# Optimization experiments

Measured on AMD Instinct MI355X. Metric: run time of the kernel, lower is better.

The kernel has to match this reference:

```python
import jax, jax.numpy as jnp
import numpy as np

B, S, D = 1, 1024, 64
_EPS = 1e-15
_BND = 1.0 - 1e-7  # artanh domain clamp (mirrors geoopt projection)


def _sq(x):
    return jnp.sum(x * x, axis=-1, keepdims=True)


def _nrm(x):
    return jnp.sqrt(_sq(x) + _EPS)


def _normalize(x, axis, eps):
    n = jnp.sqrt(jnp.sum(x * x, axis=axis, keepdims=True))
    return x / jnp.maximum(n, eps)


def _mobius_add(x, y):
    x2, y2 = _sq(x), _sq(y)
    xy = jnp.sum(x * y, axis=-1, keepdims=True)
    num = (1.0 + 2.0 * xy + y2) * x + (1.0 - x2) * y
    den = 1.0 + 2.0 * xy + x2 * y2
    return num / jnp.maximum(den, _EPS)


def _expmap0(u):
    n = _nrm(u)
    return jnp.tanh(n) * u / n


def _logmap0(y):
    n = _nrm(y)
    return jnp.arctanh(jnp.clip(n, 0.0, _BND)) * y / n


def _dist(x, y):
    n = _nrm(_mobius_add(-x, y))[..., 0]
    return 2.0 * jnp.arctanh(jnp.clip(n, 0.0, _BND))


def _logmap(x, y):
    d = _mobius_add(-x, y)
    n = _nrm(d)
    lam = 2.0 / jnp.maximum(1.0 - _sq(x), _EPS)
    return (2.0 / lam) * jnp.arctanh(jnp.clip(n, 0.0, _BND)) * d / n


def _transp0back(x, v):
    return v / jnp.maximum(1.0 - _sq(x), _EPS)


def _forward(q_in, k_in, v_in, Wq, bq, Wk, bk, Wv, bv, Wo, bo,
             tau, gamma, tangent_scale, gumbel_u, v_rand_init):
    q = q_in @ Wq.T + bq
    k = k_in @ Wk.T + bk
    v = v_in @ Wv.T + bv

    q_hyp = _expmap0(q)   # [B,S,D]
    k_hyp = _expmap0(k)

    # all-pairs geodesic distances [B,S,S]
    dist = _dist(q_hyp[:, :, None, :], k_hyp[:, None, :, :])
    min_d = jnp.min(dist, axis=-1, keepdims=True)
    w_un = jnp.exp(-(dist - min_d))                         # unnormalized weights
    w_sum = jnp.sum(w_un, axis=-1, keepdims=True) + 1e-8
    w_probs = w_un / w_sum
    h = jnp.einsum('bqk,bkd->bqd', w_probs, v)

    # Einstein midpoint: weighted Euclidean centroid of pre-map keys -> manifold
    centroid_euc = jnp.einsum('bqk,bkd->bqd', w_un / w_sum, k)
    centroid_hyp = _expmap0(centroid_euc)                   # [B,S,D]

    c2k = _dist(centroid_hyp[:, :, None, :], k_hyp[:, None, :, :])  # [B,S,S]
    wnv = w_un / w_sum
    entropy = -jnp.sum(wnv * jnp.log(wnv + 1e-8), axis=-1, keepdims=True)
    eff_mass = jnp.exp(entropy)
    variance = jnp.sum(wnv * c2k ** 2, axis=-1, keepdims=True)
    tension = variance - tau * eff_mass                     # [B,S,1]

    # matrix-free TPCA power iteration on weighted local tangents
    k_local = _logmap(centroid_hyp[:, :, None, :], k_hyp[:, None, :, :])  # [B,S,S,D]
    weighted_k = k_local * jnp.sqrt(w_un[..., None] + 1e-8)
    v_r = _normalize(v_rand_init, axis=2, eps=1e-12)        # [B,S,D,1]
    for _ in range(3):
        proj = jnp.einsum('bqkd,bqdo->bqko', weighted_k, v_r)
        v_r = jnp.einsum('bqkd,bqko->bqdo', weighted_k, proj)
        v_r = _normalize(v_r, axis=2, eps=1e-12)
    w_proj_local = v_r[..., 0]                              # [B,S,D]
    w_proj_global = _transp0back(centroid_hyp, w_proj_local)

    q_tan = _logmap0(q_hyp)
    c_tan = _logmap0(centroid_hyp)
    fallback = _normalize(q_tan - c_tan, axis=-1, eps=1e-8)
    w_proj = jnp.where(variance > 1e-5, w_proj_global, fallback)

    h_norm = _nrm(h)
    h_comp = jnp.arcsinh(h_norm) * (h / (h_norm + 1e-8))

    # Pitchfork bifurcation (c = 1)
    x = jnp.sum(h_comp * w_proj, axis=-1, keepdims=True)
    diss = (tension > 0).astype(h.dtype)
    h_mag = _nrm(h_comp)
    amplitude = h_mag * jnp.tanh(tension) * diss
    g = -jnp.log(-jnp.log(gumbel_u))                        # gumbel noise, logits = 0
    y_soft = jax.nn.softmax(g / 0.5, axis=-1)
    y_hard = jax.nn.one_hot(jnp.argmax(y_soft, axis=-1), 2, dtype=h.dtype)
    gp = y_soft + jax.lax.stop_gradient(y_hard - y_soft)    # straight-through
    eps_g = (gp[..., 0] - gp[..., 1])[..., None]            # gp @ [1,-1]
    x_star = eps_g * amplitude
    delta_c = jnp.tanh(x_star - x)
    h_prime = h_comp + delta_c * w_proj
    hp_norm = _nrm(h_prime) + 1e-8
    h_pb = h_prime * (jnp.tanh(hp_norm * tangent_scale) / hp_norm)
    h_prime_hyp = _expmap0(h_pb)

    h_out_bif = _logmap0(h_prime_hyp)
    gate = jax.nn.sigmoid(gamma)
    h_fused = (1.0 - gate) * h + gate * h_out_bif
    return h_fused @ Wo.T + bo


def setup_inputs() -> dict:
    key = jax.random.key(0)
    ks = jax.random.split(key, 10)
    std = 0.02
    return {
        'q_in': jax.random.normal(ks[0], (B, S, D), jnp.float32),
        'k_in': jax.random.normal(ks[1], (B, S, D), jnp.float32),
        'v_in': jax.random.normal(ks[2], (B, S, D), jnp.float32),
        'Wq': std * jax.random.normal(ks[3], (D, D), jnp.float32),
        'bq': jnp.zeros((D,), jnp.float32),
        'Wk': std * jax.random.normal(ks[4], (D, D), jnp.float32),
        'bk': jnp.zeros((D,), jnp.float32),
        'Wv': std * jax.random.normal(ks[5], (D, D), jnp.float32),
        'bv': jnp.zeros((D,), jnp.float32),
        'Wo': std * jax.random.normal(ks[6], (D, D), jnp.float32),
        'bo': jnp.zeros((D,), jnp.float32),
        'tau': jnp.float32(5.0),
        'gamma': jnp.float32(0.0),
        'tangent_scale': jnp.float32(0.1),
        'gumbel_u': jax.random.uniform(ks[7], (B, S, 2), jnp.float32, 1e-6, 1.0 - 1e-6),
        'v_rand_init': jax.random.normal(ks[8], (B, S, D, 1), jnp.float32),
    }


def reference(q_in, k_in, v_in, Wq, bq, Wk, bk, Wv, bv, Wo, bo,
              tau, gamma, tangent_scale, gumbel_u, v_rand_init):
    return _forward(q_in, k_in, v_in, Wq, bq, Wk, bk, Wv, bv, Wo, bo,
                    tau, gamma, tangent_scale, gumbel_u, v_rand_init)
```

## Files before the change

### kernel.cpp

```cpp
#include <hip/hip_runtime.h>
#include <hip/hip_fp16.h>
#include <math.h>

#define S 1024
#define D 64
#define BND 0.99999994f
#define FINF 3.4e38f
#define FMA4(acc,s,v) { (acc).x+=(s)*(v).x; (acc).y+=(s)*(v).y; (acc).z+=(s)*(v).z; (acc).w+=(s)*(v).w; }

__device__ __forceinline__ float waveSum(float v){
  #pragma unroll
  for(int o=32;o>0;o>>=1) v += __shfl_xor(v,o,64);
  return v;
}
__device__ __forceinline__ float2 blockSum512_v2(float2 v, float* red){
  #pragma unroll
  for(int o=32;o>0;o>>=1){ v.x+=__shfl_xor(v.x,o,64); v.y+=__shfl_xor(v.y,o,64); }
  const int wid=threadIdx.x>>6;
  __syncthreads();
  if((threadIdx.x&63)==0){ red[wid*2]=v.x; red[wid*2+1]=v.y; }
  __syncthreads();
  float2 s={0.f,0.f};
  #pragma unroll
  for(int k=0;k<8;k++){ s.x+=red[k*2]; s.y+=red[k*2+1]; }
  return s;
}
__device__ __forceinline__ float2 blockMin512_v2(float2 v, float* red){
  #pragma unroll
  for(int o=32;o>0;o>>=1){ v.x=fminf(v.x,__shfl_xor(v.x,o,64)); v.y=fminf(v.y,__shfl_xor(v.y,o,64)); }
  const int wid=threadIdx.x>>6;
  __syncthreads();
  if((threadIdx.x&63)==0){ red[wid*2]=v.x; red[wid*2+1]=v.y; }
  __syncthreads();
  float2 s={red[0],red[1]};
  #pragma unroll
  for(int k=1;k<8;k++){ s.x=fminf(s.x,red[k*2]); s.y=fminf(s.y,red[k*2+1]); }
  return s;
}
__device__ __forceinline__ float distF(float dot, float y2, float x2, float B){
  const float A=1.f-2.f*dot+y2;
  const float den=fmaxf(1.f-2.f*dot+x2*y2,1e-15f);
  const float num2=fmaxf(A*A*x2 + B*B*y2 - 2.f*A*B*dot, 0.f);
  const float nn=sqrtf(num2/(den*den)+1e-15f);
  return 2.f*atanhf(fminf(nn,BND));
}

__global__ __launch_bounds__(64) void k_proj(
  const float* __restrict__ qin, const float* __restrict__ kin, const float* __restrict__ vin,
  const float* __restrict__ Wq, const float* __restrict__ bq,
  const float* __restrict__ Wk, const float* __restrict__ bk,
  const float* __restrict__ Wv, const float* __restrict__ bv,
  const float* __restrict__ vrand,
  float* __restrict__ q_hyp, float* __restrict__ k_hyp, float* __restrict__ kT,
  __half* __restrict__ kTp,
  float* __restrict__ vproj, float* __restrict__ kproj,
  float* __restrict__ q2, float* __restrict__ k2, float* __restrict__ v_r)
{
  const int i = blockIdx.x, d = threadIdx.x;
  __shared__ __align__(16) float lq[D], lk[D], lv[D];
  __shared__ __align__(16) float skh[D];
  lq[d]=qin[i*D+d]; lk[d]=kin[i*D+d]; lv[d]=vin[i*D+d];
  __syncthreads();
  float aq=bq[d], ak=bk[d], av=bv[d];
  const float4* wq4=(const float4*)(Wq + d*D);
  const float4* wk4=(const float4*)(Wk + d*D);
  const float4* wv4=(const float4*)(Wv + d*D);
  #pragma unroll
  for(int e=0;e<16;e++){
    float4 a=wq4[e], b=wk4[e], c=wv4[e];
    aq += lq[4*e]*a.x + lq[4*e+1]*a.y + lq[4*e+2]*a.z + lq[4*e+3]*a.w;
    ak += lk[4*e]*b.x + lk[4*e+1]*b.y + lk[4*e+2]*b.z + lk[4*e+3]*b.w;
    av += lv[4*e]*c.x + lv[4*e+1]*c.y + lv[4*e+2]*c.z + lv[4*e+3]*c.w;
  }
  float nq = sqrtf(waveSum(aq*aq)+1e-15f);
  float qh = tanhf(nq)*aq/nq;
  q_hyp[i*D+d]=qh;
  float q2v = waveSum(qh*qh);
  if(d==0) q2[i]=q2v;
  float nk = sqrtf(waveSum(ak*ak)+1e-15f);
  float kh = tanhf(nk)*ak/nk;
  k_hyp[i*D+d]=kh;
  kT[(size_t)d*S + i]=kh;
  skh[d]=kh;
  float k2v = waveSum(kh*kh);
  if(d==0) k2[i]=k2v;
  vproj[i*D+d]=av;
  kproj[i*D+d]=ak;
  float vr = vrand[i*D+d];
  float nn = sqrtf(waveSum(vr*vr));
  v_r[i*D+d] = vr/fmaxf(nn,1e-12f);
  __syncthreads();
  if(d<32){
    __half2 hp=__floats2half2_rn(skh[2*d], skh[2*d+1]);
    ((__half2*)kTp)[(size_t)d*S + i]=hp;
  }
}

__global__ __launch_bounds__(512,4) void k_wc(
  const float* __restrict__ q_hyp, const float* __restrict__ kT,
  const float* __restrict__ q2a, const float* __restrict__ k2a,
  const float* __restrict__ vproj, const float* __restrict__ kproj,
  float* __restrict__ wbuf, float* __restrict__ wsum, float* __restrict__ effm,
  float* __restrict__ h, float* __restrict__ c_hyp, float* __restrict__ c2)
{
  const int i0=blockIdx.x*2, tid=threadIdx.x;
  __shared__ __align__(16) float qv[2][D];
  __shared__ __align__(16) float wl[2][S];
  __shared__ __align__(16) float4 sA[1024];
  __shared__ __align__(16) float4 sB[1024];
  __shared__ float red[16];
  if(tid<128) qv[tid>>6][tid&63]=q_hyp[i0*D+tid];
  __syncthreads();
  const float x20=q2a[i0], x21=q2a[i0+1];
  const float B0=1.f-x20, B1=1.f-x21;
  const int j0=2*tid;
  float t00=0.f,t01=0.f,t10=0.f,t11=0.f;
  #pragma unroll 8
  for(int d=0;d<64;++d){
    const float2 y=*(const float2*)(kT + (size_t)d*S + j0);
    const float c0=qv[0][d], c1=qv[1][d];
    t00+=y.x*c0; t01+=y.x*c1; t10+=y.y*c0; t11+=y.y*c1;
  }
  const float2 y2p=*(const float2*)(k2a + j0);
  const float ds00=distF(t00,y2p.x,x20,B0);
  const float ds10=distF(t10,y2p.y,x20,B0);
  const float ds01=distF(t01,y2p.x,x21,B1);
  const float ds11=distF(t11,y2p.y,x21,B1);
  float2 mn2={fminf(ds00,ds10), fminf(ds01,ds11)};
  mn2=blockMin512_v2(mn2,red);
  const float w00=expf(mn2.x-ds00), w10=expf(mn2.x-ds10);
  const float w01=expf(mn2.y-ds01), w11=expf(mn2.y-ds11);
  { float2 a={w00,w10}; *(float2*)&wl[0][j0]=a; *(float2*)(wbuf+(size_t)i0*S+j0)=a; }
  { float2 a={w01,w11}; *(float2*)&wl[1][j0]=a; *(float2*)(wbuf+(size_t)(i0+1)*S+j0)=a; }
  float2 s2={w00+w10, w01+w11};
  s2=blockSum512_v2(s2,red);
  const float s0=s2.x+1e-8f, s1=s2.y+1e-8f;
  if(tid==0){ wsum[i0]=s0; wsum[i0+1]=s1; }
  const float inv0=1.f/s0, inv1=1.f/s1;
  float2 e2={0.f,0.f};
  { const float p0=w00*inv0, p1=w10*inv0; e2.x -= p0*logf(p0+1e-8f)+p1*logf(p1+1e-8f); }
  { const float p0=w01*inv1, p1=w11*inv1; e2.y -= p0*logf(p0+1e-8f)+p1*logf(p1+1e-8f); }
  e2=blockSum512_v2(e2,red);
  if(tid==0){ effm[i0]=expf(e2.x); effm[i0+1]=expf(e2.y); }
  const int dq=tid&15, g=tid>>4;
  float* const pA=(float*)sA;
  float* const pB=(float*)sB;
  {
    float4 ah0={0,0,0,0}, ah1={0,0,0,0}, ac0={0,0,0,0}, ac1={0,0,0,0};
    #pragma unroll 4
    for(int jj=0;jj<32;jj++){
      const int j=jj*32+g;
      const float4 yv=((const float4*)(vproj + j*D))[dq];
      const float4 yk=((const float4*)(kproj + j*D))[dq];
      const float u0=wl[0][j], u1=wl[1][j];
      FMA4(ah0,u0,yv); FMA4(ah1,u1,yv);
      FMA4(ac0,u0,yk); FMA4(ac1,u1,yk);
    }
    *(float4*)&pA[(g*2+0)*64+dq*4]=ah0;
    *(float4*)&pA[(g*2+1)*64+dq*4]=ah1;
    *(float4*)&pB[(g*2+0)*64+dq*4]=ac0;
    *(float4*)&pB[(g*2+1)*64+dq*4]=ac1;
  }
  __syncthreads();
  if(tid<128){
    const int q=tid>>6, d=tid&63;
    float hs=0.f, cs=0.f;
    #pragma unroll 8
    for(int gg=0;gg<32;gg++){ hs+=pA[(gg*2+q)*64+d]; cs+=pB[(gg*2+q)*64+d]; }
    const float invq = q ? inv1 : inv0;
    h[(i0+q)*D+d]=hs*invq;
    const float ca=cs*invq;
    const float n=sqrtf(waveSum(ca*ca)+1e-15f);
    const float ch=tanhf(n)*ca/n;
    c_hyp[(i0+q)*D+d]=ch;
    const float c2v=waveSum(ch*ch);
    if(d==0) c2[i0+q]=c2v;
  }
}

__global__ __launch_bounds__(512,4) void k_pmega(
  const float* __restrict__ c_hyp, const float* __restrict__ k_hyp,
  const float* __restrict__ kT, const __half* __restrict__ kTp,
  const float* __restrict__ c2a, const float* __restrict__ k2a,
  const float* __restrict__ wbuf, const float* __restrict__ wsum,
  const float* __restrict__ effm, const float* __restrict__ tau_p,
  const float* __restrict__ h, const float* __restrict__ q_hyp,
  const float* __restrict__ q2a, const float* __restrict__ v_r,
  const float* __restrict__ gu, const float* __restrict__ gamma_p,
  const float* __restrict__ ts_p, const float* __restrict__ Wo,
  const float* __restrict__ bo, float* __restrict__ out)
{
  const int i0=blockIdx.x*2, tid=threadIdx.x;
  __shared__ __align__(16) float cv[2][D];
  __shared__ __align__(16) float vv[2][D];
  __shared__ __align__(16) float aal[2][S];
  __shared__ __align__(16) float bbl[2][S];
  __shared__ __align__(16) float prow[2][S];
  __shared__ __align__(16) float4 sA[1024];
  __shared__ __align__(16) float fus[2][D];
  __shared__ float red[16];
  __shared__ float scd[2];
  float* const pA=(float*)sA;

  if(tid<128){
    const int q=tid>>6, d=tid&63;
    const float ch=c_hyp[i0*D+tid];
    const float vr=v_r[i0*D+tid];
    cv[q][d]=ch; vv[q][d]=vr;
    const float cd=waveSum(ch*vr);
    if(d==0) scd[q]=cd;
  }
  __syncthreads();
  const float x20=c2a[i0], x21=c2a[i0+1];
  const float Bc0=1.f-x20, Bc1=1.f-x21;
  const float mB0=fmaxf(Bc0,1e-15f), mB1=fmaxf(Bc1,1e-15f);
  const float inv0=1.f/wsum[i0], inv1=1.f/wsum[i0+1];
  const int j0=2*tid;
  const int dq=tid&15, g=tid>>4;
  const float tau=tau_p[0];

  float2 var2;
  {
    float u00=0.f,u01=0.f,u10=0.f,u11=0.f;
    #pragma unroll 8
    for(int d=0;d<64;++d){
      const float2 y=*(const float2*)(kT + (size_t)d*S + j0);
      const float c0=cv[0][d], c1=cv[1][d];
      u00+=y.x*c0; u01+=y.x*c1; u10+=y.y*c0; u11+=y.y*c1;
    }
    const float2 y2p=*(const float2*)(k2a + j0);
    const float2 w0=*(const float2*)(wbuf+(size_t)i0*S+j0);
    const float2 w1=*(const float2*)(wbuf+(size_t)(i0+1)*S+j0);
    float var0=0.f, var1=0.f;
    float a00,a10,a01,a11,b00,b10,b01,b11;
    {
      const float A=1.f-2.f*u00+y2p.x;
      const float den=fmaxf(1.f-2.f*u00+x20*y2p.x,1e-15f);
      const float num2=fmaxf(A*A*x20+Bc0*Bc0*y2p.x-2.f*A*Bc0*u00,0.f);
      const float nn=sqrtf(num2/(den*den)+1e-15f);
      const float art=atanhf(fminf(nn,BND));
      var0 += w0.x*inv0*4.f*art*art;
      const float coef=sqrtf(w0.x+1e-8f)*mB0*art/(nn*den);
      a00=-coef*A; b00=coef*Bc0;
    }
    {
      const float A=1.f-2.f*u10+y2p.y;
      const float den=fmaxf(1.f-2.f*u10+x20*y2p.y,1e-15f);
      const float num2=fmaxf(A*A*x20+Bc0*Bc0*y2p.y-2.f*A*Bc0*u10,0.f);
      const float nn=sqrtf(num2/(den*den)+1e-15f);
      const float art=atanhf(fminf(nn,BND));
      var0 += w0.y*inv0*4.f*art*art;
      const float coef=sqrtf(w0.y+1e-8f)*mB0*art/(nn*den);
      a10=-coef*A; b10=coef*Bc0;
    }
    {
      const float A=1.f-2.f*u01+y2p.x;
      const float den=fmaxf(1.f-2.f*u01+x21*y2p.x,1e-15f);
      const float num2=fmaxf(A*A*x21+Bc1*Bc1*y2p.x-2.f*A*Bc1*u01,0.f);
      const float nn=sqrtf(num2/(den*den)+1e-15f);
      const float art=atanhf(fminf(nn,BND));
      var1 += w1.x*inv1*4.f*art*art;
      const float coef=sqrtf(w1.x+1e-8f)*mB1*art/(nn*den);
      a01=-coef*A; b01=coef*Bc1;
    }
    {
      const float A=1.f-2.f*u11+y2p.y;
      const float den=fmaxf(1.f-2.f*u11+x21*y2p.y,1e-15f);
      const float num2=fmaxf(A*A*x21+Bc1*Bc1*y2p.y-2.f*A*Bc1*u11,0.f);
      const float nn=sqrtf(num2/(den*den)+1e-15f);
      const float art=atanhf(fminf(nn,BND));
      var1 += w1.y*inv1*4.f*art*art;
      const float coef=sqrtf(w1.y+1e-8f)*mB1*art/(nn*den);
      a11=-coef*A; b11=coef*Bc1;
    }
    { float2 t={a00,a10}; *(float2*)&aal[0][j0]=t; }
    { float2 t={a01,a11}; *(float2*)&aal[1][j0]=t; }
    { float2 t={b00,b10}; *(float2*)&bbl[0][j0]=t; }
    { float2 t={b01,b11}; *(float2*)&bbl[1][j0]=t; }
    float2 v2={var0,var1};
    var2=blockSum512_v2(v2,red);
  }

  float2 sal2;
  for(int it3=0; it3<3; ++it3){
    float t00=0.f,t01=0.f,t10=0.f,t11=0.f;
    #pragma unroll 8
    for(int dp=0;dp<32;++dp){
      const __half2 h0=((const __half2*)kTp)[(size_t)dp*S + j0];
      const __half2 h1=((const __half2*)kTp)[(size_t)dp*S + j0+1];
      const float2 f0=__half22float2(h0);
      const float2 f1=__half22float2(h1);
      const float2 v0=*(const float2*)&vv[0][2*dp];
      const float2 v1=*(const float2*)&vv[1][2*dp];
      t00 += f0.x*v0.x + f0.y*v0.y;
      t01 += f0.x*v1.x + f0.y*v1.y;
      t10 += f1.x*v0.x + f1.y*v0.y;
      t11 += f1.x*v1.x + f1.y*v1.y;
    }
    {
      const float cd0=scd[0], cd1=scd[1];
      const float2 a0=*(const float2*)&aal[0][j0], b0=*(const float2*)&bbl[0][j0];
      const float2 a1=*(const float2*)&aal[1][j0], b1=*(const float2*)&bbl[1][j0];
      const float p00=a0.x*cd0+b0.x*t00, p10=a0.y*cd0+b0.y*t10;
      const float p01=a1.x*cd1+b1.x*t01, p11=a1.y*cd1+b1.y*t11;
      { float2 t={p00*b0.x, p10*b0.y}; *(float2*)&prow[0][j0]=t; }
      { float2 t={p01*b1.x, p11*b1.y}; *(float2*)&prow[1][j0]=t; }
      float2 s={p00*a0.x+p10*a0.y, p01*a1.x+p11*a1.y};
      sal2=blockSum512_v2(s,red);
    }
    {
      float4 a0={0,0,0,0}, a1={0,0,0,0};
      #pragma unroll 4
      for(int jj=0;jj<32;jj++){
        const int j=jj*32+g;
        const float4 y=((const float4*)(k_hyp + j*D))[dq];
        const float u0=prow[0][j], u1=prow[1][j];
        FMA4(a0,u0,y); FMA4(a1,u1,y);
      }
      *(float4*)&pA[(g*2+0)*64+dq*4]=a0;
      *(float4*)&pA[(g*2+1)*64+dq*4]=a1;
    }
    __syncthreads();
    if(tid<128){
      const int q=tid>>6, d=tid&63;
      float od=(q?sal2.y:sal2.x)*cv[q][d];
      #pragma unroll 8
      for(int gg=0;gg<32;gg++) od += pA[(gg*2+q)*64+d];
      const float nn=sqrtf(waveSum(od*od));
      const float vn=od/fmaxf(nn,1e-12f);
      vv[q][d]=vn;
      const float cd=waveSum(cv[q][d]*vn);
      if(d==0) scd[q]=cd;
    }
    __syncthreads();
  }

  if(tid<128){
    const int q=tid>>6, d=tid&63;
    const int i=i0+q;
    const float vart = q ? var2.y : var2.x;
    const float tns = vart - tau*effm[i];
    const float x2q_c = q ? x21 : x20;
    const float vd=vv[q][d];
    const float hd=h[i*D+d];
    const float qd=q_hyp[i*D+d];
    const float q2=q2a[i];
    const float wpg=vd/fmaxf(1.f-x2q_c,1e-15f);
    const float nq=sqrtf(q2+1e-15f);
    const float qt=atanhf(fminf(nq,BND))*qd/nq;
    const float ncn=sqrtf(x2q_c+1e-15f);
    const float ct=atanhf(fminf(ncn,BND))*cv[q][d]/ncn;
    const float df=qt-ct;
    const float nd=sqrtf(waveSum(df*df));
    const float fb=df/fmaxf(nd,1e-8f);
    const float wp=(vart>1e-5f)?wpg:fb;
    const float hn=sqrtf(waveSum(hd*hd)+1e-15f);
    const float hc=asinhf(hn)*hd/(hn+1e-8f);
    const float x=waveSum(hc*wp);
    const float hmag=sqrtf(waveSum(hc*hc)+1e-15f);
    const float amp=(tns>0.f)? hmag*tanhf(tns) : 0.f;
    const float u0=gu[i*2], u1=gu[i*2+1];
    const float eg=(u0>=u1)?1.f:-1.f;
    const float dc=tanhf(eg*amp - x);
    const float hp=hc+dc*wp;
    const float hpn=sqrtf(waveSum(hp*hp)+1e-15f)+1e-8f;
    const float hpb=hp*(tanhf(hpn*ts_p[0])/hpn);
    const float n2=sqrtf(waveSum(hpb*hpb)+1e-15f);
    const float hyp=tanhf(n2)*hpb/n2;
    const float n3=sqrtf(waveSum(hyp*hyp)+1e-15f);
    const float bif=atanhf(fminf(n3,BND))*hyp/n3;
    const float gate=1.f/(1.f+expf(-gamma_p[0]));
    fus[q][d]=(1.f-gate)*hd + gate*bif;
  }
  __syncthreads();
  if(tid<128){
    const int q=tid>>6, d=tid&63;
    float acc=bo[d];
    const float4* wo4=(const float4*)(Wo + d*D);
    #pragma unroll
    for(int e=0;e<16;e++){
      float4 wv=wo4[e];
      acc += fus[q][4*e]*wv.x + fus[q][4*e+1]*wv.y + fus[q][4*e+2]*wv.z + fus[q][4*e+3]*wv.w;
    }
    out[(i0+q)*D+d]=acc;
  }
}

extern "C" void kernel_launch(void* const* d_in, const int* in_sizes, int n_in,
                              void* d_out, int out_size, void* d_ws, size_t ws_size,
                              hipStream_t stream)
{
  const float* qin=(const float*)d_in[0];
  const float* kin=(const float*)d_in[1];
  const float* vin=(const float*)d_in[2];
  const float* Wq=(const float*)d_in[3];
  const float* bq=(const float*)d_in[4];
  const float* Wk=(const float*)d_in[5];
  const float* bk=(const float*)d_in[6];
  const float* Wv=(const float*)d_in[7];
  const float* bv=(const float*)d_in[8];
  const float* Wo=(const float*)d_in[9];
  const float* bo=(const float*)d_in[10];
  const float* tau=(const float*)d_in[11];
  const float* gamma=(const float*)d_in[12];
  const float* tscale=(const float*)d_in[13];
  const float* gu=(const float*)d_in[14];
  const float* vrand=(const float*)d_in[15];
  float* out=(float*)d_out;

  float* p=(float*)d_ws;
  float* q_hyp=p; p+=S*D;
  float* k_hyp=p; p+=S*D;
  float* kT=p;    p+=S*D;
  float* vproj=p; p+=S*D;
  float* kproj=p; p+=S*D;
  float* v_r=p;   p+=S*D;
  float* h=p;     p+=S*D;
  float* c_hyp=p; p+=S*D;
  float* q2=p;   p+=S;
  float* k2=p;   p+=S;
  float* c2=p;   p+=S;
  float* wsum=p; p+=S;
  float* effm=p; p+=S;
  __half* kTp=(__half*)p; p+=(S*D)/2;
  float* wbuf=p; p+=(size_t)S*S;

  k_proj<<<S,64,0,stream>>>(qin,kin,vin,Wq,bq,Wk,bk,Wv,bv,vrand,
                            q_hyp,k_hyp,kT,kTp,vproj,kproj,q2,k2,v_r);
  k_wc<<<S/2,512,0,stream>>>(q_hyp,kT,q2,k2,vproj,kproj,
                             wbuf,wsum,effm,h,c_hyp,c2);
  k_pmega<<<S/2,512,0,stream>>>(c_hyp,k_hyp,kT,kTp,c2,k2,wbuf,wsum,effm,tau,
                                h,q_hyp,q2,v_r,gu,gamma,tscale,Wo,bo,out);
}
```

Before: 82.55 us.

## Use 1024-thread blocks with one key per thread and interleave v/k projections

Doubles the block size of the weight/centroid and main kernels so that each thread handles one key column instead of two, which doubles the number of waves per query pair and the parallelism available to hide latency. The v and k projections are stored interleaved in one 128-wide buffer, so the weighted-sum pass reads both with one float4 stream and needs one shared reduction buffer. The cost is more reduction partials, more shared memory per block, and heavier register pressure under the 1024-thread launch bound.

```diff
diff --git a/kernel.cpp b/kernel.cpp
--- a/kernel.cpp
+++ b/kernel.cpp
@@ -13,7 +13,7 @@
   for(int o=32;o>0;o>>=1) v += __shfl_xor(v,o,64);
   return v;
 }
-__device__ __forceinline__ float2 blockSum512_v2(float2 v, float* red){
+__device__ __forceinline__ float2 blockSum1024_v2(float2 v, float* red){
   #pragma unroll
   for(int o=32;o>0;o>>=1){ v.x+=__shfl_xor(v.x,o,64); v.y+=__shfl_xor(v.y,o,64); }
   const int wid=threadIdx.x>>6;
@@ -22,10 +22,10 @@
   __syncthreads();
   float2 s={0.f,0.f};
   #pragma unroll
-  for(int k=0;k<8;k++){ s.x+=red[k*2]; s.y+=red[k*2+1]; }
+  for(int k=0;k<16;k++){ s.x+=red[k*2]; s.y+=red[k*2+1]; }
   return s;
 }
-__device__ __forceinline__ float2 blockMin512_v2(float2 v, float* red){
+__device__ __forceinline__ float2 blockMin1024_v2(float2 v, float* red){
   #pragma unroll
   for(int o=32;o>0;o>>=1){ v.x=fminf(v.x,__shfl_xor(v.x,o,64)); v.y=fminf(v.y,__shfl_xor(v.y,o,64)); }
   const int wid=threadIdx.x>>6;
@@ -34,7 +34,7 @@
   __syncthreads();
   float2 s={red[0],red[1]};
   #pragma unroll
-  for(int k=1;k<8;k++){ s.x=fminf(s.x,red[k*2]); s.y=fminf(s.y,red[k*2+1]); }
+  for(int k=1;k<16;k++){ s.x=fminf(s.x,red[k*2]); s.y=fminf(s.y,red[k*2+1]); }
   return s;
 }
 __device__ __forceinline__ float distF(float dot, float y2, float x2, float B){
@@ -52,8 +52,7 @@
   const float* __restrict__ Wv, const float* __restrict__ bv,
   const float* __restrict__ vrand,
   float* __restrict__ q_hyp, float* __restrict__ k_hyp, float* __restrict__ kT,
-  __half* __restrict__ kTp,
-  float* __restrict__ vproj, float* __restrict__ kproj,
+  __half* __restrict__ kTp, float* __restrict__ vk,
   float* __restrict__ q2, float* __restrict__ k2, float* __restrict__ v_r)
 {
   const int i = blockIdx.x, d = threadIdx.x;
@@ -84,8 +83,8 @@
   skh[d]=kh;
   float k2v = waveSum(kh*kh);
   if(d==0) k2[i]=k2v;
-  vproj[i*D+d]=av;
-  kproj[i*D+d]=ak;
+  vk[(size_t)i*128 + d]      = av;
+  vk[(size_t)i*128 + 64 + d] = ak;
   float vr = vrand[i*D+d];
   float nn = sqrtf(waveSum(vr*vr));
   v_r[i*D+d] = vr/fmaxf(nn,1e-12f);
@@ -96,89 +95,84 @@
   }
 }
 
-__global__ __launch_bounds__(512,4) void k_wc(
+__global__ __launch_bounds__(1024,8) void k_wc(
   const float* __restrict__ q_hyp, const float* __restrict__ kT,
   const float* __restrict__ q2a, const float* __restrict__ k2a,
-  const float* __restrict__ vproj, const float* __restrict__ kproj,
+  const float* __restrict__ vk,
   float* __restrict__ wbuf, float* __restrict__ wsum, float* __restrict__ effm,
   float* __restrict__ h, float* __restrict__ c_hyp, float* __restrict__ c2)
 {
   const int i0=blockIdx.x*2, tid=threadIdx.x;
   __shared__ __align__(16) float qv[2][D];
   __shared__ __align__(16) float wl[2][S];
-  __shared__ __align__(16) float4 sA[1024];
-  __shared__ __align__(16) float4 sB[1024];
-  __shared__ float red[16];
+  __shared__ __align__(16) float4 sA[2048];
+  __shared__ float red[32];
   if(tid<128) qv[tid>>6][tid&63]=q_hyp[i0*D+tid];
   __syncthreads();
   const float x20=q2a[i0], x21=q2a[i0+1];
   const float B0=1.f-x20, B1=1.f-x21;
-  const int j0=2*tid;
-  float t00=0.f,t01=0.f,t10=0.f,t11=0.f;
+  const int j=tid;
+  float t0=0.f, t1=0.f;
   #pragma unroll 8
   for(int d=0;d<64;++d){
-    const float2 y=*(const float2*)(kT + (size_t)d*S + j0);
-    const float c0=qv[0][d], c1=qv[1][d];
-    t00+=y.x*c0; t01+=y.x*c1; t10+=y.y*c0; t11+=y.y*c1;
-  }
-  const float2 y2p=*(const float2*)(k2a + j0);
-  const float ds00=distF(t00,y2p.x,x20,B0);
-  const float ds10=distF(t10,y2p.y,x20,B0);
-  const float ds01=distF(t01,y2p.x,x21,B1);
-  const float ds11=distF(t11,y2p.y,x21,B1);
-  float2 mn2={fminf(ds00,ds10), fminf(ds01,ds11)};
-  mn2=blockMin512_v2(mn2,red);
-  const float w00=expf(mn2.x-ds00), w10=expf(mn2.x-ds10);
-  const float w01=expf(mn2.y-ds01), w11=expf(mn2.y-ds11);
-  { float2 a={w00,w10}; *(float2*)&wl[0][j0]=a; *(float2*)(wbuf+(size_t)i0*S+j0)=a; }
-  { float2 a={w01,w11}; *(float2*)&wl[1][j0]=a; *(float2*)(wbuf+(size_t)(i0+1)*S+j0)=a; }
-  float2 s2={w00+w10, w01+w11};
-  s2=blockSum512_v2(s2,red);
+    const float y=kT[(size_t)d*S + j];
+    t0+=y*qv[0][d]; t1+=y*qv[1][d];
+  }
+  const float y2=k2a[j];
+  const float ds0=distF(t0,y2,x20,B0);
+  const float ds1=distF(t1,y2,x21,B1);
+  float2 mn2={ds0,ds1};
+  mn2=blockMin1024_v2(mn2,red);
+  const float w0=expf(mn2.x-ds0);
+  const float w1=expf(mn2.y-ds1);
+  wl[0][j]=w0; wl[1][j]=w1;
+  wbuf[(size_t)i0*S+j]=w0; wbuf[(size_t)(i0+1)*S+j]=w1;
+  float2 s2={w0,w1};
+  s2=blockSum1024_v2(s2,red);
   const float s0=s2.x+1e-8f, s1=s2.y+1e-8f;
   if(tid==0){ wsum[i0]=s0; wsum[i0+1]=s1; }
   const float inv0=1.f/s0, inv1=1.f/s1;
-  float2 e2={0.f,0.f};
-  { const float p0=w00*inv0, p1=w10*inv0; e2.x -= p0*logf(p0+1e-8f)+p1*logf(p1+1e-8f); }
-  { const float p0=w01*inv1, p1=w11*inv1; e2.y -= p0*logf(p0+1e-8f)+p1*logf(p1+1e-8f); }
-  e2=blockSum512_v2(e2,red);
+  float2 e2;
+  { const float p0=w0*inv0, p1=w1*inv1;
+    e2.x = -p0*logf(p0+1e-8f);
+    e2.y = -p1*logf(p1+1e-8f); }
+  e2=blockSum1024_v2(e2,red);
   if(tid==0){ effm[i0]=expf(e2.x); effm[i0+1]=expf(e2.y); }
-  const int dq=tid&15, g=tid>>4;
+  const int dq5=tid&31, g=tid>>5;
   float* const pA=(float*)sA;
-  float* const pB=(float*)sB;
   {
-    float4 ah0={0,0,0,0}, ah1={0,0,0,0}, ac0={0,0,0,0}, ac1={0,0,0,0};
+    float4 a0={0,0,0,0}, a1={0,0,0,0};
     #pragma unroll 4
     for(int jj=0;jj<32;jj++){
-      const int j=jj*32+g;
-      const float4 yv=((const float4*)(vproj + j*D))[dq];
-      const float4 yk=((const float4*)(kproj + j*D))[dq];
-      const float u0=wl[0][j], u1=wl[1][j];
-      FMA4(ah0,u0,yv); FMA4(ah1,u1,yv);
-      FMA4(ac0,u0,yk); FMA4(ac1,u1,yk);
-    }
-    *(float4*)&pA[(g*2+0)*64+dq*4]=ah0;
-    *(float4*)&pA[(g*2+1)*64+dq*4]=ah1;
-    *(float4*)&pB[(g*2+0)*64+dq*4]=ac0;
-    *(float4*)&pB[(g*2+1)*64+dq*4]=ac1;
-  }
-  __syncthreads();
-  if(tid<128){
-    const int q=tid>>6, d=tid&63;
-    float hs=0.f, cs=0.f;
+      const int j2=jj*32+g;
+      const float4 y=((const float4*)(vk + (size_t)j2*128))[dq5];
+      const float u0=wl[0][j2], u1=wl[1][j2];
+      FMA4(a0,u0,y); FMA4(a1,u1,y);
+    }
+    *(float4*)&pA[(g*2+0)*128 + dq5*4]=a0;
+    *(float4*)&pA[(g*2+1)*128 + dq5*4]=a1;
+  }
+  __syncthreads();
+  if(tid<256){
+    const int q=tid>>7, dd=tid&127;
+    float s=0.f;
     #pragma unroll 8
-    for(int gg=0;gg<32;gg++){ hs+=pA[(gg*2+q)*64+d]; cs+=pB[(gg*2+q)*64+d]; }
-    const float invq = q ? inv1 : inv0;
-    h[(i0+q)*D+d]=hs*invq;
-    const float ca=cs*invq;
-    const float n=sqrtf(waveSum(ca*ca)+1e-15f);
-    const float ch=tanhf(n)*ca/n;
-    c_hyp[(i0+q)*D+d]=ch;
-    const float c2v=waveSum(ch*ch);
-    if(d==0) c2[i0+q]=c2v;
-  }
-}
-
-__global__ __launch_bounds__(512,4) void k_pmega(
+    for(int gg=0;gg<32;gg++) s+=pA[(gg*2+q)*128+dd];
+    s *= (q ? inv1 : inv0);
+    if(dd<64){
+      h[(i0+q)*D+dd]=s;
+    }else{
+      const int d=dd-64;
+      const float n=sqrtf(waveSum(s*s)+1e-15f);
+      const float ch=tanhf(n)*s/n;
+      c_hyp[(i0+q)*D+d]=ch;
+      const float c2v=waveSum(ch*ch);
+      if(d==0) c2[i0+q]=c2v;
+    }
+  }
+}
+
+__global__ __launch_bounds__(1024,8) void k_pmega(
   const float* __restrict__ c_hyp, const float* __restrict__ k_hyp,
   const float* __restrict__ kT, const __half* __restrict__ kTp,
   const float* __restrict__ c2a, const float* __restrict__ k2a,
@@ -196,9 +190,9 @@
   __shared__ __align__(16) float aal[2][S];
   __shared__ __align__(16) float bbl[2][S];
   __shared__ __align__(16) float prow[2][S];
-  __shared__ __align__(16) float4 sA[1024];
+  __shared__ __align__(16) float4 sA[2048];
   __shared__ __align__(16) float fus[2][D];
-  __shared__ float red[16];
+  __shared__ float red[32];
   __shared__ float scd[2];
   float* const pA=(float*)sA;
 
@@ -215,106 +209,76 @@
   const float Bc0=1.f-x20, Bc1=1.f-x21;
   const float mB0=fmaxf(Bc0,1e-15f), mB1=fmaxf(Bc1,1e-15f);
   const float inv0=1.f/wsum[i0], inv1=1.f/wsum[i0+1];
-  const int j0=2*tid;
+  const int j=tid;
   const int dq=tid&15, g=tid>>4;
   const float tau=tau_p[0];
 
   float2 var2;
   {
-    float u00=0.f,u01=0.f,u10=0.f,u11=0.f;
+    float u0=0.f, u1=0.f;
     #pragma unroll 8
     for(int d=0;d<64;++d){
-      const float2 y=*(const float2*)(kT + (size_t)d*S + j0);
-      const float c0=cv[0][d], c1=cv[1][d];
-      u00+=y.x*c0; u01+=y.x*c1; u10+=y.y*c0; u11+=y.y*c1;
-    }
-    const float2 y2p=*(const float2*)(k2a + j0);
-    const float2 w0=*(const float2*)(wbuf+(size_t)i0*S+j0);
-    const float2 w1=*(const float2*)(wbuf+(size_t)(i0+1)*S+j0);
-    float var0=0.f, var1=0.f;
-    float a00,a10,a01,a11,b00,b10,b01,b11;
+      const float y=kT[(size_t)d*S + j];
+      u0+=y*cv[0][d]; u1+=y*cv[1][d];
+    }
+    const float y2=k2a[j];
+    const float wq0=wbuf[(size_t)i0*S+j];
+    const float wq1=wbuf[(size_t)(i0+1)*S+j];
+    float var0, var1;
     {
-      const float A=1.f-2.f*u00+y2p.x;
-      const float den=fmaxf(1.f-2.f*u00+x20*y2p.x,1e-15f);
-      const float num2=fmaxf(A*A*x20+Bc0*Bc0*y2p.x-2.f*A*Bc0*u00,0.f);
+      const float A=1.f-2.f*u0+y2;
+      const float den=fmaxf(1.f-2.f*u0+x20*y2,1e-15f);
+      const float num2=fmaxf(A*A*x20+Bc0*Bc0*y2-2.f*A*Bc0*u0,0.f);
       const float nn=sqrtf(num2/(den*den)+1e-15f);
       const float art=atanhf(fminf(nn,BND));
-      var0 += w0.x*inv0*4.f*art*art;
-      const float coef=sqrtf(w0.x+1e-8f)*mB0*art/(nn*den);
-      a00=-coef*A; b00=coef*Bc0;
+      var0 = wq0*inv0*4.f*art*art;
+      const float coef=sqrtf(wq0+1e-8f)*mB0*art/(nn*den);
+      aal[0][j]=-coef*A; bbl[0][j]=coef*Bc0;
     }
     {
-      const float A=1.f-2.f*u10+y2p.y;
-      const float den=fmaxf(1.f-2.f*u10+x20*y2p.y,1e-15f);
-      const float num2=fmaxf(A*A*x20+Bc0*Bc0*y2p.y-2.f*A*Bc0*u10,0.f);
+      const float A=1.f-2.f*u1+y2;
+      const float den=fmaxf(1.f-2.f*u1+x21*y2,1e-15f);
+      const float num2=fmaxf(A*A*x21+Bc1*Bc1*y2-2.f*A*Bc1*u1,0.f);
       const float nn=sqrtf(num2/(den*den)+1e-15f);
       const float art=atanhf(fminf(nn,BND));
-      var0 += w0.y*inv0*4.f*art*art;
-      const float coef=sqrtf(w0.y+1e-8f)*mB0*art/(nn*den);
-      a10=-coef*A; b10=coef*Bc0;
-    }
-    {
-      const float A=1.f-2.f*u01+y2p.x;
-      const float den=fmaxf(1.f-2.f*u01+x21*y2p.x,1e-15f);
-      const float num2=fmaxf(A*A*x21+Bc1*Bc1*y2p.x-2.f*A*Bc1*u01,0.f);
-      const float nn=sqrtf(num2/(den*den)+1e-15f);
-      const float art=atanhf(fminf(nn,BND));
-      var1 += w1.x*inv1*4.f*art*art;
-      const float coef=sqrtf(w1.x+1e-8f)*mB1*art/(nn*den);
-      a01=-coef*A; b01=coef*Bc1;
-    }
-    {
-      const float A=1.f-2.f*u11+y2p.y;
-      const float den=fmaxf(1.f-2.f*u11+x21*y2p.y,1e-15f);
-      const float num2=fmaxf(A*A*x21+Bc1*Bc1*y2p.y-2.f*A*Bc1*u11,0.f);
-      const float nn=sqrtf(num2/(den*den)+1e-15f);
-      const float art=atanhf(fminf(nn,BND));
-      var1 += w1.y*inv1*4.f*art*art;
-      const float coef=sqrtf(w1.y+1e-8f)*mB1*art/(nn*den);
-      a11=-coef*A; b11=coef*Bc1;
-    }
-    { float2 t={a00,a10}; *(float2*)&aal[0][j0]=t; }
-    { float2 t={a01,a11}; *(float2*)&aal[1][j0]=t; }
-    { float2 t={b00,b10}; *(float2*)&bbl[0][j0]=t; }
-    { float2 t={b01,b11}; *(float2*)&bbl[1][j0]=t; }
+      var1 = wq1*inv1*4.f*art*art;
+      const float coef=sqrtf(wq1+1e-8f)*mB1*art/(nn*den);
+      aal[1][j]=-coef*A; bbl[1][j]=coef*Bc1;
+    }
     float2 v2={var0,var1};
-    var2=blockSum512_v2(v2,red);
+    var2=blockSum1024_v2(v2,red);
   }
 
   float2 sal2;
   for(int it3=0; it3<3; ++it3){
-    float t00=0.f,t01=0.f,t10=0.f,t11=0.f;
+    float t0=0.f, t1=0.f;
     #pragma unroll 8
     for(int dp=0;dp<32;++dp){
-      const __half2 h0=((const __half2*)kTp)[(size_t)dp*S + j0];
-      const __half2 h1=((const __half2*)kTp)[(size_t)dp*S + j0+1];
-      const float2 f0=__half22float2(h0);
-      const float2 f1=__half22float2(h1);
+      const __half2 hy=((const __half2*)kTp)[(size_t)dp*S + j];
+      const float2 f=__half22float2(hy);
       const float2 v0=*(const float2*)&vv[0][2*dp];
       const float2 v1=*(const float2*)&vv[1][2*dp];
-      t00 += f0.x*v0.x + f0.y*v0.y;
-      t01 += f0.x*v1.x + f0.y*v1.y;
-      t10 += f1.x*v0.x + f1.y*v0.y;
-      t11 += f1.x*v1.x + f1.y*v1.y;
+      t0 += f.x*v0.x + f.y*v0.y;
+      t1 += f.x*v1.x + f.y*v1.y;
     }
     {
       const float cd0=scd[0], cd1=scd[1];
-      const float2 a0=*(const float2*)&aal[0][j0], b0=*(const float2*)&bbl[0][j0];
-      const float2 a1=*(const float2*)&aal[1][j0], b1=*(const float2*)&bbl[1][j0];
-      const float p00=a0.x*cd0+b0.x*t00, p10=a0.y*cd0+b0.y*t10;
-      const float p01=a1.x*cd1+b1.x*t01, p11=a1.y*cd1+b1.y*t11;
-      { float2 t={p00*b0.x, p10*b0.y}; *(float2*)&prow[0][j0]=t; }
-      { float2 t={p01*b1.x, p11*b1.y}; *(float2*)&prow[1][j0]=t; }
-      float2 s={p00*a0.x+p10*a0.y, p01*a1.x+p11*a1.y};
-      sal2=blockSum512_v2(s,red);
+      const float a0=aal[0][j], b0=bbl[0][j];
+      const float a1=aal[1][j], b1=bbl[1][j];
+      const float p0=a0*cd0+b0*t0;
+      const float p1=a1*cd1+b1*t1;
+      prow[0][j]=p0*b0;
+      prow[1][j]=p1*b1;
+      float2 s={p0*a0, p1*a1};
+      sal2=blockSum1024_v2(s,red);
     }
     {
       float4 a0={0,0,0,0}, a1={0,0,0,0};
       #pragma unroll 4
-      for(int jj=0;jj<32;jj++){
-        const int j=jj*32+g;
-        const float4 y=((const float4*)(k_hyp + j*D))[dq];
-        const float u0=prow[0][j], u1=prow[1][j];
+      for(int jj=0;jj<16;jj++){
+        const int j2=jj*64+g;
+        const float4 y=((const float4*)(k_hyp + j2*D))[dq];
+        const float u0=prow[0][j2], u1=prow[1][j2];
         FMA4(a0,u0,y); FMA4(a1,u1,y);
       }
       *(float4*)&pA[(g*2+0)*64+dq*4]=a0;
@@ -325,7 +289,7 @@
       const int q=tid>>6, d=tid&63;
       float od=(q?sal2.y:sal2.x)*cv[q][d];
       #pragma unroll 8
-      for(int gg=0;gg<32;gg++) od += pA[(gg*2+q)*64+d];
+      for(int gg=0;gg<64;gg++) od += pA[(gg*2+q)*64+d];
       const float nn=sqrtf(waveSum(od*od));
       const float vn=od/fmaxf(nn,1e-12f);
       vv[q][d]=vn;
@@ -412,8 +376,7 @@
   float* q_hyp=p; p+=S*D;
   float* k_hyp=p; p+=S*D;
   float* kT=p;    p+=S*D;
-  float* vproj=p; p+=S*D;
-  float* kproj=p; p+=S*D;
+  float* vk=p;    p+=(size_t)S*128;
   float* v_r=p;   p+=S*D;
   float* h=p;     p+=S*D;
   float* c_hyp=p; p+=S*D;
@@ -426,9 +389,9 @@
   float* wbuf=p; p+=(size_t)S*S;
 
   k_proj<<<S,64,0,stream>>>(qin,kin,vin,Wq,bq,Wk,bk,Wv,bv,vrand,
-                            q_hyp,k_hyp,kT,kTp,vproj,kproj,q2,k2,v_r);
-  k_wc<<<S/2,512,0,stream>>>(q_hyp,kT,q2,k2,vproj,kproj,
-                             wbuf,wsum,effm,h,c_hyp,c2);
-  k_pmega<<<S/2,512,0,stream>>>(c_hyp,k_hyp,kT,kTp,c2,k2,wbuf,wsum,effm,tau,
-                                h,q_hyp,q2,v_r,gu,gamma,tscale,Wo,bo,out);
-}
+                            q_hyp,k_hyp,kT,kTp,vk,q2,k2,v_r);
+  k_wc<<<S/2,1024,0,stream>>>(q_hyp,kT,q2,k2,vk,
+                              wbuf,wsum,effm,h,c_hyp,c2);
+  k_pmega<<<S/2,1024,0,stream>>>(c_hyp,k_hyp,kT,kTp,c2,k2,wbuf,wsum,effm,tau,
+                                 h,q_hyp,q2,v_r,gu,gamma,tscale,Wo,bo,out);
+}
```

Result: slower. 108.7 us (+31.7%).
